# Kernel tuning notes

Measured on AMD Instinct MI355X. Metric: run time of the kernel, lower is better.

Reference implementation:

```python
import jax, jax.numpy as jnp
import numpy as np

NEG_BIG = -9.0e15  # mask value used by the torch module
LEAKY_SLOPE = 0.01  # torch nn.LeakyReLU default


def setup_inputs() -> dict:
    key = jax.random.key(0)
    k1, k2, k3, k4 = jax.random.split(key, 4)
    N, F_in, F_out = 8192, 256, 128
    x = jax.random.normal(k1, (N, F_in), dtype=jnp.float32)
    adj = jax.random.randint(k2, (N, N), 0, 2, dtype=jnp.int32)
    W = jax.random.normal(k3, (F_in, F_out), dtype=jnp.float32) * 0.05
    a = jax.random.normal(k4, (2 * F_out, 1), dtype=jnp.float32) * 0.05
    return {"x": x, "adj": adj, "W": W, "a": a}


def reference(x, adj, W, a):
    F_out = W.shape[1]
    h = x @ W                                   # [N, F_out]
    # e[i, j] = leaky_relu([h_i || h_j] . a) = leaky_relu(h_i.a1 + h_j.a2)
    a1, a2 = a[:F_out, 0], a[F_out:, 0]
    e = h @ a1[:, None] + (h @ a2)[None, :]     # [N, N]
    e = jax.nn.leaky_relu(e, negative_slope=LEAKY_SLOPE)
    scores = jnp.where(adj > 0, e, NEG_BIG)
    attention = jax.nn.softmax(scores, axis=1)  # dropout p=0 -> identity
    h1 = jax.nn.elu(attention @ h)              # [N, F_out]
    return h1, attention
```

## Files before the change

### kernel.cpp

```cpp
#include <hip/hip_runtime.h>

#define N 8192
#define FI 256
#define FO 128

typedef short bf16x8 __attribute__((ext_vector_type(8)));
typedef float f32x4 __attribute__((ext_vector_type(4)));
typedef unsigned short u16x4 __attribute__((ext_vector_type(4)));
typedef unsigned long long u64;
typedef u64 u64x2 __attribute__((ext_vector_type(2)));

static __device__ __forceinline__ unsigned short f2bf(float x) {
  unsigned int u = __builtin_bit_cast(unsigned int, x);
  u = (u + 0x7fffu + ((u >> 16) & 1u)) >> 16;
  return (unsigned short)u;
}
static __device__ __forceinline__ float lrelu(float x) {
  return fmaxf(x, 0.01f * x);
}
static __device__ __forceinline__ void barrier_lds() {
  asm volatile("s_waitcnt lgkmcnt(0)" ::: "memory");
  __builtin_amdgcn_s_barrier();
  asm volatile("" ::: "memory");
}

__global__ __launch_bounds__(256) void k_prep(
    const float* __restrict__ x, const float* __restrict__ W, const float* __restrict__ a,
    unsigned short* __restrict__ h_t, float* __restrict__ ha1, float* __restrict__ ha2) {
  __shared__ float xs[16][256];
  __shared__ float redA[16][2], redB[16][2];
  const int t = threadIdx.x;
  const int i0 = blockIdx.x * 16;
  #pragma unroll
  for (int ii = 0; ii < 16; ++ii)
    xs[ii][t & 255] = x[(long long)(i0 + ii) * FI + t];
  __syncthreads();
  const int rg = t >> 7;
  const int f = t & 127;
  float accs[8] = {0.f, 0.f, 0.f, 0.f, 0.f, 0.f, 0.f, 0.f};
  for (int k = 0; k < 256; ++k) {
    const float wv = W[k * FO + f];
    #pragma unroll
    for (int rr = 0; rr < 8; ++rr) accs[rr] = fmaf(xs[rg * 8 + rr][k], wv, accs[rr]);
  }
  {
    ushort4 s0, s1;
    s0.x = f2bf(accs[0]); s0.y = f2bf(accs[1]); s0.z = f2bf(accs[2]); s0.w = f2bf(accs[3]);
    s1.x = f2bf(accs[4]); s1.y = f2bf(accs[5]); s1.z = f2bf(accs[6]); s1.w = f2bf(accs[7]);
    unsigned short* dst = h_t + (long long)f * N + i0 + rg * 8;
    *(ushort4*)dst = s0;
    *(ushort4*)(dst + 4) = s1;
  }
  const float a1f = a[f];
  const float a2f = a[FO + f];
  const int lane = t & 63;
  const int wig = (t >> 6) & 1;
  #pragma unroll
  for (int rr = 0; rr < 8; ++rr) {
    float v1 = accs[rr] * a1f;
    float v2 = accs[rr] * a2f;
    #pragma unroll
    for (int off = 32; off; off >>= 1) { v1 += __shfl_xor(v1, off); v2 += __shfl_xor(v2, off); }
    if (lane == 0) { redA[rg * 8 + rr][wig] = v1; redB[rg * 8 + rr][wig] = v2; }
  }
  __syncthreads();
  if (t < 16) {
    ha1[i0 + t] = redA[t][0] + redA[t][1];
    ha2[i0 + t] = redB[t][0] + redB[t][1];
  }
}

template <int WM>
__global__ __launch_bounds__(256) void k_mask(
    const int* __restrict__ adj, const float* __restrict__ ha1g, const float* __restrict__ ha2g,
    u64* __restrict__ msk, float* __restrict__ lse_row) {
  __shared__ float h2s[N];
  const int t = threadIdx.x;
  const int lane = t & 63;
  #pragma unroll
  for (int i = 0; i < 8; ++i) {
    const int idx = i * 1024 + t * 4;
    *(float4*)&h2s[idx] = *(const float4*)(ha2g + idx);
  }
  __syncthreads();
  const int row = blockIdx.x * 4 + (t >> 6);
  const float ei = ha1g[row];
  const int* __restrict__ arow = adj + (size_t)row * N;
  u64* __restrict__ mrow = msk + (size_t)row * 128;
  unsigned int bits0 = 0, bits1 = 0, bits2 = 0, bits3 = 0;
  float mloc = -3.0e38f;
  for (int it = 0; it < 32; ++it) {
    const int j0 = it * 256 + lane * 4;
    const int4 a4 = *(const int4*)(arow + j0);
    const float4 h2 = *(const float4*)&h2s[j0];
    const bool b0 = a4.x > 0, b1 = a4.y > 0, b2 = a4.z > 0, b3 = a4.w > 0;
    bits0 |= (b0 ? 1u : 0u) << it;
    bits1 |= (b1 ? 1u : 0u) << it;
    bits2 |= (b2 ? 1u : 0u) << it;
    bits3 |= (b3 ? 1u : 0u) << it;
    mloc = fmaxf(mloc, b0 ? h2.x : -3.0e38f);
    mloc = fmaxf(mloc, b1 ? h2.y : -3.0e38f);
    mloc = fmaxf(mloc, b2 ? h2.z : -3.0e38f);
    mloc = fmaxf(mloc, b3 ? h2.w : -3.0e38f);
    if (WM) {
      const u64 q0 = __ballot(b0), q1 = __ballot(b1);
      const u64 q2 = __ballot(b2), q3 = __ballot(b3);
      if (lane == 0) {
        u64x2 v01 = {q0, q1}, v23 = {q2, q3};
        *(u64x2*)(mrow + it * 4) = v01;
        *(u64x2*)(mrow + it * 4 + 2) = v23;
      }
    }
  }
  #pragma unroll
  for (int off = 32; off; off >>= 1) mloc = fmaxf(mloc, __shfl_xor(mloc, off));
  const float m = lrelu(ei + mloc);
  float s0 = 0.f, s1 = 0.f, s2 = 0.f, s3 = 0.f;
  for (int it = 0; it < 32; ++it) {
    const int j0 = it * 256 + lane * 4;
    const float4 h2 = *(const float4*)&h2s[j0];
    s0 += ((bits0 >> it) & 1) ? __expf(lrelu(ei + h2.x) - m) : 0.f;
    s1 += ((bits1 >> it) & 1) ? __expf(lrelu(ei + h2.y) - m) : 0.f;
    s2 += ((bits2 >> it) & 1) ? __expf(lrelu(ei + h2.z) - m) : 0.f;
    s3 += ((bits3 >> it) & 1) ? __expf(lrelu(ei + h2.w) - m) : 0.f;
  }
  float s = (s0 + s1) + (s2 + s3);
  #pragma unroll
  for (int off = 32; off; off >>= 1) s += __shfl_xor(s, off);
  if (lane == 0) lse_row[row] = (s > 0.f) ? (m + __logf(s)) : 3.0e38f;
}

template <int UA>
__global__ __launch_bounds__(512) void k_pv(
    const int* __restrict__ adj, const u64* __restrict__ msk,
    const unsigned short* __restrict__ h_t, const float* __restrict__ ha1g,
    const float* __restrict__ ha2g, const float* __restrict__ lse_row,
    float* __restrict__ h1, float* __restrict__ attn) {
  __shared__ unsigned short p_lds[2][16][136];
  const int t = threadIdx.x;
  const int lane = t & 63;
  const int w = t >> 6;
  const int base = blockIdx.x * 16;
  const int pr = t >> 5;
  const int pjw = t & 31;
  const float ei = ha1g[base + pr];
  const float nls = lse_row[base + pr];
  const u64* __restrict__ mrow = msk + (size_t)(base + pr) * 128;
  const int* __restrict__ arow = adj + (size_t)(base + pr) * N;
  float* __restrict__ atrow = attn + (size_t)(base + pr) * N;

  const int f0 = w * 16;
  const unsigned short* __restrict__ hbase =
      h_t + (size_t)(f0 + (lane & 15)) * N + (lane >> 4) * 8;
  const unsigned short* pfrag0 = &p_lds[0][lane & 15][(lane >> 4) * 8];

  f32x4 acc = {0.f, 0.f, 0.f, 0.f};

  auto compute_p = [&](int jt) {
    const int j = jt * 128 + pjw * 4;
    bool b0, b1, b2, b3;
    if constexpr (UA) {
      const int4 a4 = *(const int4*)(arow + j);
      b0 = a4.x > 0; b1 = a4.y > 0; b2 = a4.z > 0; b3 = a4.w > 0;
    } else {
      const int it = j >> 8;
      const int l = (j >> 2) & 63;
      const u64x2 qa = *(const u64x2*)(mrow + it * 4);
      const u64x2 qb = *(const u64x2*)(mrow + it * 4 + 2);
      b0 = (qa.x >> l) & 1; b1 = (qa.y >> l) & 1;
      b2 = (qb.x >> l) & 1; b3 = (qb.y >> l) & 1;
    }
    const float4 h2 = *(const float4*)(ha2g + j);
    const float p0 = b0 ? __expf(lrelu(ei + h2.x) - nls) : 0.f;
    const float p1 = b1 ? __expf(lrelu(ei + h2.y) - nls) : 0.f;
    const float p2 = b2 ? __expf(lrelu(ei + h2.z) - nls) : 0.f;
    const float p3 = b3 ? __expf(lrelu(ei + h2.w) - nls) : 0.f;
    f32x4 pv = {p0, p1, p2, p3};
    __builtin_nontemporal_store(pv, (f32x4*)(atrow + j));
    u16x4 pb = {f2bf(p0), f2bf(p1), f2bf(p2), f2bf(p3)};
    *(u16x4*)&p_lds[(jt & 1)][pr][pjw * 4] = pb;
  };

  bf16x8 hA[4], hB[4];
  compute_p(0);
  #pragma unroll
  for (int ks = 0; ks < 4; ++ks) hA[ks] = *(const bf16x8*)(hbase + ks * 32);
  barrier_lds();

  for (int jt = 0; jt < 64; ++jt) {
    if (jt < 63) {
      compute_p(jt + 1);
      #pragma unroll
      for (int ks = 0; ks < 4; ++ks)
        hB[ks] = *(const bf16x8*)(hbase + (jt + 1) * 128 + ks * 32);
    }
    const unsigned short* pf = pfrag0 + (jt & 1) * (16 * 136);
    #pragma unroll
    for (int ks = 0; ks < 4; ++ks) {
      const bf16x8 av = *(const bf16x8*)(pf + ks * 32);
      acc = __builtin_amdgcn_mfma_f32_16x16x32_bf16(av, hA[ks], acc, 0, 0, 0);
    }
    if (jt < 63) {
      barrier_lds();
      #pragma unroll
      for (int ks = 0; ks < 4; ++ks) hA[ks] = hB[ks];
    }
  }
  {
    const int rbase = (lane >> 4) * 4;
    const int col = lane & 15;
    #pragma unroll
    for (int rgi = 0; rgi < 4; ++rgi) {
      float v = acc[rgi];
      v = v > 0.f ? v : __expf(v) - 1.f;
      h1[(long long)(base + rbase + rgi) * FO + f0 + col] = v;
    }
  }
}

extern "C" void kernel_launch(void* const* d_in, const int* in_sizes, int n_in,
                              void* d_out, int out_size, void* d_ws, size_t ws_size,
                              hipStream_t stream) {
  const float* x = (const float*)d_in[0];
  const int* adj = (const int*)d_in[1];
  const float* W = (const float*)d_in[2];
  const float* a = (const float*)d_in[3];
  float* h1 = (float*)d_out;
  float* attn = (float*)d_out + (size_t)N * FO;

  char* wsb = (char*)d_ws;
  unsigned short* h_t = (unsigned short*)wsb;
  float* ha1 = (float*)(wsb + (size_t)FO * N * 2);
  float* ha2 = ha1 + N;
  float* lse = ha2 + N;
  const size_t msk_off = (size_t)FO * N * 2 + 3 * (size_t)N * 4;
  u64* msk = (u64*)(wsb + msk_off);
  const size_t need = msk_off + (size_t)N * 128 * 8;

  k_prep<<<N / 16, 256, 0, stream>>>(x, W, a, h_t, ha1, ha2);
  if (ws_size >= need) {
    k_mask<1><<<N / 4, 256, 0, stream>>>(adj, ha1, ha2, msk, lse);
    k_pv<0><<<N / 16, 512, 0, stream>>>(adj, msk, h_t, ha1, ha2, lse, h1, attn);
  } else {
    k_mask<0><<<N / 4, 256, 0, stream>>>(adj, ha1, ha2, msk, lse);
    k_pv<1><<<N / 16, 512, 0, stream>>>(adj, msk, h_t, ha1, ha2, lse, h1, attn);
  }
}
```

Measured before the change: 271.0 us.

## Halve k_pv block to 256 threads with two MFMA tiles per wave, drop LDS staging in k_mask

```diff
diff --git a/kernel.cpp b/kernel.cpp
--- a/kernel.cpp
+++ b/kernel.cpp
@@ -6,7 +6,6 @@
 
 typedef short bf16x8 __attribute__((ext_vector_type(8)));
 typedef float f32x4 __attribute__((ext_vector_type(4)));
-typedef unsigned short u16x4 __attribute__((ext_vector_type(4)));
 typedef unsigned long long u64;
 typedef u64 u64x2 __attribute__((ext_vector_type(2)));
 
@@ -17,11 +16,6 @@
 }
 static __device__ __forceinline__ float lrelu(float x) {
   return fmaxf(x, 0.01f * x);
-}
-static __device__ __forceinline__ void barrier_lds() {
-  asm volatile("s_waitcnt lgkmcnt(0)" ::: "memory");
-  __builtin_amdgcn_s_barrier();
-  asm volatile("" ::: "memory");
 }
 
 __global__ __launch_bounds__(256) void k_prep(
@@ -74,34 +68,27 @@
 __global__ __launch_bounds__(256) void k_mask(
     const int* __restrict__ adj, const float* __restrict__ ha1g, const float* __restrict__ ha2g,
     u64* __restrict__ msk, float* __restrict__ lse_row) {
-  __shared__ float h2s[N];
   const int t = threadIdx.x;
   const int lane = t & 63;
-  #pragma unroll
-  for (int i = 0; i < 8; ++i) {
-    const int idx = i * 1024 + t * 4;
-    *(float4*)&h2s[idx] = *(const float4*)(ha2g + idx);
-  }
-  __syncthreads();
   const int row = blockIdx.x * 4 + (t >> 6);
   const float ei = ha1g[row];
   const int* __restrict__ arow = adj + (size_t)row * N;
   u64* __restrict__ mrow = msk + (size_t)row * 128;
   unsigned int bits0 = 0, bits1 = 0, bits2 = 0, bits3 = 0;
-  float mloc = -3.0e38f;
+  float m0 = -3.0e38f, m1 = -3.0e38f, m2 = -3.0e38f, m3 = -3.0e38f;
   for (int it = 0; it < 32; ++it) {
     const int j0 = it * 256 + lane * 4;
     const int4 a4 = *(const int4*)(arow + j0);
-    const float4 h2 = *(const float4*)&h2s[j0];
+    const float4 h2 = *(const float4*)(ha2g + j0);
     const bool b0 = a4.x > 0, b1 = a4.y > 0, b2 = a4.z > 0, b3 = a4.w > 0;
     bits0 |= (b0 ? 1u : 0u) << it;
     bits1 |= (b1 ? 1u : 0u) << it;
     bits2 |= (b2 ? 1u : 0u) << it;
     bits3 |= (b3 ? 1u : 0u) << it;
-    mloc = fmaxf(mloc, b0 ? h2.x : -3.0e38f);
-    mloc = fmaxf(mloc, b1 ? h2.y : -3.0e38f);
-    mloc = fmaxf(mloc, b2 ? h2.z : -3.0e38f);
-    mloc = fmaxf(mloc, b3 ? h2.w : -3.0e38f);
+    m0 = fmaxf(m0, b0 ? h2.x : -3.0e38f);
+    m1 = fmaxf(m1, b1 ? h2.y : -3.0e38f);
+    m2 = fmaxf(m2, b2 ? h2.z : -3.0e38f);
+    m3 = fmaxf(m3, b3 ? h2.w : -3.0e38f);
     if (WM) {
       const u64 q0 = __ballot(b0), q1 = __ballot(b1);
       const u64 q2 = __ballot(b2), q3 = __ballot(b3);
@@ -112,13 +99,14 @@
       }
     }
   }
+  float mloc = fmaxf(fmaxf(m0, m1), fmaxf(m2, m3));
   #pragma unroll
   for (int off = 32; off; off >>= 1) mloc = fmaxf(mloc, __shfl_xor(mloc, off));
   const float m = lrelu(ei + mloc);
   float s0 = 0.f, s1 = 0.f, s2 = 0.f, s3 = 0.f;
   for (int it = 0; it < 32; ++it) {
     const int j0 = it * 256 + lane * 4;
-    const float4 h2 = *(const float4*)&h2s[j0];
+    const float4 h2 = *(const float4*)(ha2g + j0);
     s0 += ((bits0 >> it) & 1) ? __expf(lrelu(ei + h2.x) - m) : 0.f;
     s1 += ((bits1 >> it) & 1) ? __expf(lrelu(ei + h2.y) - m) : 0.f;
     s2 += ((bits2 >> it) & 1) ? __expf(lrelu(ei + h2.z) - m) : 0.f;
@@ -131,7 +119,7 @@
 }
 
 template <int UA>
-__global__ __launch_bounds__(512) void k_pv(
+__global__ __launch_bounds__(256, 4) void k_pv(
     const int* __restrict__ adj, const u64* __restrict__ msk,
     const unsigned short* __restrict__ h_t, const float* __restrict__ ha1g,
     const float* __restrict__ ha2g, const float* __restrict__ lse_row,
@@ -141,69 +129,95 @@
   const int lane = t & 63;
   const int w = t >> 6;
   const int base = blockIdx.x * 16;
-  const int pr = t >> 5;
-  const int pjw = t & 31;
+  const int pr = t >> 4;
+  const int pjw = t & 15;
   const float ei = ha1g[base + pr];
   const float nls = lse_row[base + pr];
   const u64* __restrict__ mrow = msk + (size_t)(base + pr) * 128;
   const int* __restrict__ arow = adj + (size_t)(base + pr) * N;
   float* __restrict__ atrow = attn + (size_t)(base + pr) * N;
 
-  const int f0 = w * 16;
-  const unsigned short* __restrict__ hbase =
+  const int f0 = w * 32;
+  const unsigned short* __restrict__ hb0 =
       h_t + (size_t)(f0 + (lane & 15)) * N + (lane >> 4) * 8;
+  const unsigned short* __restrict__ hb1 = hb0 + (size_t)16 * N;
   const unsigned short* pfrag0 = &p_lds[0][lane & 15][(lane >> 4) * 8];
 
-  f32x4 acc = {0.f, 0.f, 0.f, 0.f};
+  f32x4 acc0 = {0.f, 0.f, 0.f, 0.f};
+  f32x4 acc1 = {0.f, 0.f, 0.f, 0.f};
 
   auto compute_p = [&](int jt) {
-    const int j = jt * 128 + pjw * 4;
-    bool b0, b1, b2, b3;
+    const int j0 = jt * 128 + pjw * 8;
+    unsigned int bits8;
     if constexpr (UA) {
-      const int4 a4 = *(const int4*)(arow + j);
-      b0 = a4.x > 0; b1 = a4.y > 0; b2 = a4.z > 0; b3 = a4.w > 0;
+      const int4 a0 = *(const int4*)(arow + j0);
+      const int4 a1 = *(const int4*)(arow + j0 + 4);
+      bits8 = (a0.x > 0 ? 1u : 0u) | (a0.y > 0 ? 2u : 0u) | (a0.z > 0 ? 4u : 0u) |
+              (a0.w > 0 ? 8u : 0u) | (a1.x > 0 ? 16u : 0u) | (a1.y > 0 ? 32u : 0u) |
+              (a1.z > 0 ? 64u : 0u) | (a1.w > 0 ? 128u : 0u);
     } else {
-      const int it = j >> 8;
-      const int l = (j >> 2) & 63;
+      const int it = j0 >> 8;
+      const int l = (j0 >> 2) & 63;
       const u64x2 qa = *(const u64x2*)(mrow + it * 4);
       const u64x2 qb = *(const u64x2*)(mrow + it * 4 + 2);
-      b0 = (qa.x >> l) & 1; b1 = (qa.y >> l) & 1;
-      b2 = (qb.x >> l) & 1; b3 = (qb.y >> l) & 1;
-    }
-    const float4 h2 = *(const float4*)(ha2g + j);
-    const float p0 = b0 ? __expf(lrelu(ei + h2.x) - nls) : 0.f;
-    const float p1 = b1 ? __expf(lrelu(ei + h2.y) - nls) : 0.f;
-    const float p2 = b2 ? __expf(lrelu(ei + h2.z) - nls) : 0.f;
-    const float p3 = b3 ? __expf(lrelu(ei + h2.w) - nls) : 0.f;
-    f32x4 pv = {p0, p1, p2, p3};
-    __builtin_nontemporal_store(pv, (f32x4*)(atrow + j));
-    u16x4 pb = {f2bf(p0), f2bf(p1), f2bf(p2), f2bf(p3)};
-    *(u16x4*)&p_lds[(jt & 1)][pr][pjw * 4] = pb;
+      const unsigned int n0 = (unsigned int)((qa.x >> l) & 3ull);
+      const unsigned int n1 = (unsigned int)((qa.y >> l) & 3ull);
+      const unsigned int n2 = (unsigned int)((qb.x >> l) & 3ull);
+      const unsigned int n3 = (unsigned int)((qb.y >> l) & 3ull);
+      bits8 = (n0 & 1u) | ((n1 & 1u) << 1) | ((n2 & 1u) << 2) | ((n3 & 1u) << 3) |
+              ((n0 >> 1) << 4) | ((n1 >> 1) << 5) | ((n2 >> 1) << 6) | ((n3 >> 1) << 7);
+    }
+    const float4 hA = *(const float4*)(ha2g + j0);
+    const float4 hB = *(const float4*)(ha2g + j0 + 4);
+    float p[8];
+    p[0] = (bits8 & 1u)   ? __expf(lrelu(ei + hA.x) - nls) : 0.f;
+    p[1] = (bits8 & 2u)   ? __expf(lrelu(ei + hA.y) - nls) : 0.f;
+    p[2] = (bits8 & 4u)   ? __expf(lrelu(ei + hA.z) - nls) : 0.f;
+    p[3] = (bits8 & 8u)   ? __expf(lrelu(ei + hA.w) - nls) : 0.f;
+    p[4] = (bits8 & 16u)  ? __expf(lrelu(ei + hB.x) - nls) : 0.f;
+    p[5] = (bits8 & 32u)  ? __expf(lrelu(ei + hB.y) - nls) : 0.f;
+    p[6] = (bits8 & 64u)  ? __expf(lrelu(ei + hB.z) - nls) : 0.f;
+    p[7] = (bits8 & 128u) ? __expf(lrelu(ei + hB.w) - nls) : 0.f;
+    f32x4 pv0 = {p[0], p[1], p[2], p[3]};
+    f32x4 pv1 = {p[4], p[5], p[6], p[7]};
+    __builtin_nontemporal_store(pv0, (f32x4*)(atrow + j0));
+    __builtin_nontemporal_store(pv1, (f32x4*)(atrow + j0 + 4));
+    ushort4 pb0, pb1;
+    pb0.x = f2bf(p[0]); pb0.y = f2bf(p[1]); pb0.z = f2bf(p[2]); pb0.w = f2bf(p[3]);
+    pb1.x = f2bf(p[4]); pb1.y = f2bf(p[5]); pb1.z = f2bf(p[6]); pb1.w = f2bf(p[7]);
+    *(ushort4*)&p_lds[(jt & 1)][pr][pjw * 8] = pb0;
+    *(ushort4*)&p_lds[(jt & 1)][pr][pjw * 8 + 4] = pb1;
   };
 
-  bf16x8 hA[4], hB[4];
+  bf16x8 hC0[4], hC1[4], hN0[4], hN1[4];
   compute_p(0);
   #pragma unroll
-  for (int ks = 0; ks < 4; ++ks) hA[ks] = *(const bf16x8*)(hbase + ks * 32);
-  barrier_lds();
+  for (int ks = 0; ks < 4; ++ks) {
+    hC0[ks] = *(const bf16x8*)(hb0 + ks * 32);
+    hC1[ks] = *(const bf16x8*)(hb1 + ks * 32);
+  }
+  __syncthreads();
 
   for (int jt = 0; jt < 64; ++jt) {
     if (jt < 63) {
       compute_p(jt + 1);
       #pragma unroll
-      for (int ks = 0; ks < 4; ++ks)
-        hB[ks] = *(const bf16x8*)(hbase + (jt + 1) * 128 + ks * 32);
+      for (int ks = 0; ks < 4; ++ks) {
+        hN0[ks] = *(const bf16x8*)(hb0 + (jt + 1) * 128 + ks * 32);
+        hN1[ks] = *(const bf16x8*)(hb1 + (jt + 1) * 128 + ks * 32);
+      }
     }
     const unsigned short* pf = pfrag0 + (jt & 1) * (16 * 136);
     #pragma unroll
     for (int ks = 0; ks < 4; ++ks) {
       const bf16x8 av = *(const bf16x8*)(pf + ks * 32);
-      acc = __builtin_amdgcn_mfma_f32_16x16x32_bf16(av, hA[ks], acc, 0, 0, 0);
+      acc0 = __builtin_amdgcn_mfma_f32_16x16x32_bf16(av, hC0[ks], acc0, 0, 0, 0);
+      acc1 = __builtin_amdgcn_mfma_f32_16x16x32_bf16(av, hC1[ks], acc1, 0, 0, 0);
     }
     if (jt < 63) {
-      barrier_lds();
+      __syncthreads();
       #pragma unroll
-      for (int ks = 0; ks < 4; ++ks) hA[ks] = hB[ks];
+      for (int ks = 0; ks < 4; ++ks) { hC0[ks] = hN0[ks]; hC1[ks] = hN1[ks]; }
     }
   }
   {
@@ -211,9 +225,12 @@
     const int col = lane & 15;
     #pragma unroll
     for (int rgi = 0; rgi < 4; ++rgi) {
-      float v = acc[rgi];
+      float v = acc0[rgi];
       v = v > 0.f ? v : __expf(v) - 1.f;
       h1[(long long)(base + rbase + rgi) * FO + f0 + col] = v;
+      float u = acc1[rgi];
+      u = u > 0.f ? u : __expf(u) - 1.f;
+      h1[(long long)(base + rbase + rgi) * FO + f0 + 16 + col] = u;
     }
   }
 }
@@ -240,9 +257,9 @@
   k_prep<<<N / 16, 256, 0, stream>>>(x, W, a, h_t, ha1, ha2);
   if (ws_size >= need) {
     k_mask<1><<<N / 4, 256, 0, stream>>>(adj, ha1, ha2, msk, lse);
-    k_pv<0><<<N / 16, 512, 0, stream>>>(adj, msk, h_t, ha1, ha2, lse, h1, attn);
+    k_pv<0><<<N / 16, 256, 0, stream>>>(adj, msk, h_t, ha1, ha2, lse, h1, attn);
   } else {
     k_mask<0><<<N / 4, 256, 0, stream>>>(adj, ha1, ha2, msk, lse);
-    k_pv<1><<<N / 16, 512, 0, stream>>>(adj, msk, h_t, ha1, ha2, lse, h1, attn);
-  }
-}
+    k_pv<1><<<N / 16, 256, 0, stream>>>(adj, msk, h_t, ha1, ha2, lse, h1, attn);
+  }
+}
```

After: 263.8 us. 2.7% less time.
